# Performance work log

Hardware: AMD Instinct MI355X
Metric: run time of the kernel (lower is better)

## Reference

```python
import jax, jax.numpy as jnp
import numpy as np

N, M, NNZ, N_C, D = 4096, 4096, 262144, 4, 128
ADD_RATIO, TEMP = 0.1, 0.5


def setup_inputs() -> dict:
    key = jax.random.key(0)
    ks = jax.random.split(key, 6)
    X = jax.random.normal(ks[0], (N, D), dtype=jnp.float32)
    V = jax.random.randint(ks[1], (NNZ,), 0, N)
    E = jax.random.randint(ks[2], (NNZ,), 0, M)
    # incidence matrix consistent with the (V, E) pairs
    H = jnp.zeros((N, M), jnp.float32).at[V, E].set(1.0)
    incident_mask_prob = jax.random.uniform(ks[3], (N, M), jnp.float32, 1e-4, 1.0 - 1e-4)
    cos_weight = jax.random.normal(ks[4], (N_C, D), dtype=jnp.float32)
    eps = jax.random.uniform(ks[5], (N, M), jnp.float32, 1e-6, 1.0 - 1e-6)
    return {"X": X, "H": H, "V": V, "E": E,
            "incident_mask_prob": incident_mask_prob,
            "cos_weight": cos_weight, "eps": eps}


def _l2norm(x):
    # F.normalize(p=2, dim=-1): x / max(||x||, 1e-12)
    return x / jnp.maximum(jnp.linalg.norm(x, axis=-1, keepdims=True), 1e-12)


def reference(X, H, V, E, incident_mask_prob, cos_weight, eps):
    # scatter-mean of node embeddings into edge embeddings: eX [M, D]
    counts = jax.ops.segment_sum(jnp.ones((NNZ,), X.dtype), E, num_segments=M)
    eX = jax.ops.segment_sum(X[V], E, num_segments=M) / jnp.maximum(counts, 1.0)[:, None]

    node_fc = _l2norm(X[:, None, :] * cos_weight[None])   # [N, C, D]
    edge_fc = _l2norm(eX[:, None, :] * cos_weight[None])  # [M, C, D]
    # mean over C of per-channel cosine sims -> S [N, M]
    S = jnp.einsum('ncd,mcd->nm', node_fc, edge_fc) / N_C
    S = S.at[V, E].set(-1e30)  # mask existing incidences

    num_add = max(1, int(ADD_RATIO * NNZ))
    _, idx = jax.lax.top_k(S.reshape(-1), num_add)
    row = idx // M
    col = idx % M
    delta_H = jnp.zeros_like(H).at[row, col].set(1.0)
    enriched_H = H + delta_H

    # gumbel-sigmoid with straight-through estimator
    logit = (jnp.log(eps) - jnp.log(1.0 - eps)
             + jnp.log(incident_mask_prob + 1e-8)
             - jnp.log(1.0 - incident_mask_prob + 1e-8))
    soft = jax.nn.sigmoid(logit / TEMP)
    hard = (soft > 0.5).astype(soft.dtype)
    incident_mask = hard - jax.lax.stop_gradient(soft) + soft
    return enriched_H * incident_mask
```

## Files before the change

### kernel.cpp

```cpp
#include <hip/hip_runtime.h>

#define N_NODES 4096
#define M_EDGES 4096
#define NNZ_K   262144
#define NCH     4
#define DIM     128
#define KDIM    512
#define NM      (N_NODES * M_EDGES)
#define NUM_ADD 26214
#define NCB     2048
#define NFB     32768
#define CAP     262144
#define CAP2    65536

#define EXD_OFF   0ull
#define AFC_OFF   4194304ull
#define BFC_OFF   8388608ull
#define BKT_OFF   12582912ull
#define CVAL_OFF  13631488ull
#define CIDX_OFF  15728640ull
#define CIDX2_OFF 16777216ull
#define CNT_OFF   17039360ull
#define OFFS_OFF  17055744ull
#define CUR_OFF   17072132ull
#define HIST_OFF  17088516ull
#define FHIST_OFF 17096708ull
#define SCL_OFF   17227780ull
#define ZERO_BYTES (17227844ull - CNT_OFF)
#define NINV_OFF  17227904ull
#define EINV_OFF  17358976ull

typedef short bf16x8 __attribute__((ext_vector_type(8)));
typedef float f32x4  __attribute__((ext_vector_type(4)));

#define GLOAD_LDS16(gsrc, ldst)                                                 \
    __builtin_amdgcn_global_load_lds(                                           \
        (const __attribute__((address_space(1))) void*)(gsrc),                  \
        (__attribute__((address_space(3))) void*)(ldst), 16, 0, 0)

__device__ __forceinline__ int bin_c(float s) {
    int b = (int)floorf((s + 1.0f) * 1024.0f);
    return min(max(b, 0), NCB - 1);
}

__device__ __forceinline__ int fbin_of(double v, int bstar) {
    double lo = (double)(bstar - 12) * (2.0 / 2048.0) - 1.0;
    double wd = (28.0 * (2.0 / 2048.0)) / (double)NFB;
    int f = (int)floor((v - lo) / wd);
    return min(max(f, 0), NFB - 1);
}

__device__ __forceinline__ float hard_mask(float p, float e) {
    float logit = logf(e) - logf(1.0f - e) + logf(p + 1e-8f) - logf(1.0f - p + 1e-8f);
    float soft  = 1.0f / (1.0f + expf(-2.0f * logit));
    return (soft > 0.5f) ? 1.0f : 0.0f;
}

__device__ __forceinline__ unsigned short to_bf16_rtne(float f) {
    unsigned int b = __float_as_uint(f);
    b += 0x7FFFu + ((b >> 16) & 1u);
    return (unsigned short)(b >> 16);
}

__global__ void k_count(const int* __restrict__ E, int* __restrict__ cnt) {
    int k = blockIdx.x * 256 + threadIdx.x;
    if (k < NNZ_K) atomicAdd(&cnt[E[k]], 1);
}

__global__ __launch_bounds__(256) void k_scan(const int* __restrict__ cnt, int* __restrict__ offs) {
    __shared__ int part[256];
    int t = threadIdx.x;
    int loc[16]; int s = 0;
    for (int j = 0; j < 16; ++j) { loc[j] = cnt[t * 16 + j]; s += loc[j]; }
    part[t] = s;
    __syncthreads();
    if (t == 0) { int acc = 0; for (int i = 0; i < 256; ++i) { int v = part[i]; part[i] = acc; acc += v; } }
    __syncthreads();
    int acc = part[t];
    for (int j = 0; j < 16; ++j) { offs[t * 16 + j] = acc; acc += loc[j]; }
    if (t == 255) offs[4096] = acc;
}

__global__ void k_fill(const int* __restrict__ E, const int* __restrict__ offs,
                       int* __restrict__ cur, int* __restrict__ bkt) {
    int k = blockIdx.x * 256 + threadIdx.x;
    if (k < NNZ_K) {
        int e = E[k];
        int pos = atomicAdd(&cur[e], 1);
        bkt[offs[e] + pos] = k;
    }
}

__global__ __launch_bounds__(128) void k_edge_mean(
        const int* __restrict__ Vv, const int* __restrict__ cnt,
        const int* __restrict__ offs, const int* __restrict__ bkt,
        const float* __restrict__ X, double* __restrict__ eXd) {
    __shared__ int sk[1024];
    __shared__ int sv[1024];
    int m = blockIdx.x;
    int c = cnt[m]; if (c > 1024) c = 1024;
    int off = offs[m];
    for (int t = threadIdx.x; t < c; t += 128) sk[t] = bkt[off + t];
    __syncthreads();
    for (int t = threadIdx.x; t < c; t += 128) {
        int key = sk[t]; int r = 0;
        for (int j = 0; j < c; ++j) r += (sk[j] < key);
        sv[r] = Vv[key];
    }
    __syncthreads();
    int d = threadIdx.x;
    double s = 0.0;
    for (int j = 0; j < c; ++j) s += (double)X[sv[j] * DIM + d];
    eXd[m * DIM + d] = s / (double)(c > 1 ? c : 1);
}

template <typename T>
__global__ __launch_bounds__(128) void k_fc(const T* __restrict__ in,
                                            const float* __restrict__ w,
                                            unsigned short* __restrict__ out,
                                            double* __restrict__ dinv) {
    __shared__ double red[128];
    int n = blockIdx.x, d = threadIdx.x;
    double x = (double)in[n * DIM + d];
    for (int c = 0; c < NCH; ++c) {
        double v = x * (double)w[c * DIM + d];
        red[d] = v * v;
        __syncthreads();
        for (int s = 64; s > 0; s >>= 1) { if (d < s) red[d] += red[d + s]; __syncthreads(); }
        double denom = fmax(sqrt(red[0]), 1e-12);
        __syncthreads();
        out[n * KDIM + c * DIM + d] = to_bf16_rtne((float)(v / denom));
        if (d == 0) dinv[n * NCH + c] = 1.0 / denom;
    }
}

__global__ __launch_bounds__(256) void k_gemm_mfma(const unsigned short* __restrict__ A,
                                                   const unsigned short* __restrict__ B,
                                                   float* __restrict__ S) {
    __shared__ short As[128][32];
    __shared__ short Bs[128][32];
    int tid = threadIdx.x;
    int row0 = blockIdx.y * 128, col0 = blockIdx.x * 128;
    int w = tid >> 6, l = tid & 63;
    int wr = (w >> 1) * 64, wc = (w & 1) * 64;
    f32x4 acc[4][4] = {};
    int lrow = l >> 2, lcol = (l & 3) * 8;
    int rb0 = (w * 2 + 0) * 16, rb1 = (w * 2 + 1) * 16;
    const unsigned short* sA0 = A + (size_t)(row0 + rb0 + lrow) * KDIM + lcol;
    const unsigned short* sA1 = A + (size_t)(row0 + rb1 + lrow) * KDIM + lcol;
    const unsigned short* sB0 = B + (size_t)(col0 + rb0 + lrow) * KDIM + lcol;
    const unsigned short* sB1 = B + (size_t)(col0 + rb1 + lrow) * KDIM + lcol;
    for (int k0 = 0; k0 < KDIM; k0 += 32) {
        __syncthreads();
        GLOAD_LDS16(sA0 + k0, &As[rb0][0]);
        GLOAD_LDS16(sA1 + k0, &As[rb1][0]);
        GLOAD_LDS16(sB0 + k0, &Bs[rb0][0]);
        GLOAD_LDS16(sB1 + k0, &Bs[rb1][0]);
        __syncthreads();
        int kq = (l >> 4) * 8;
        bf16x8 af[4], bfr[4];
        #pragma unroll
        for (int m = 0; m < 4; ++m) af[m] = *(const bf16x8*)&As[wr + m * 16 + (l & 15)][kq];
        #pragma unroll
        for (int n = 0; n < 4; ++n) bfr[n] = *(const bf16x8*)&Bs[wc + n * 16 + (l & 15)][kq];
        #pragma unroll
        for (int m = 0; m < 4; ++m)
            #pragma unroll
            for (int n = 0; n < 4; ++n)
                acc[m][n] = __builtin_amdgcn_mfma_f32_16x16x32_bf16(af[m], bfr[n], acc[m][n], 0, 0, 0);
    }
    #pragma unroll
    for (int m = 0; m < 4; ++m) {
        int r = row0 + wr + m * 16 + (l >> 4) * 4;
        #pragma unroll
        for (int n = 0; n < 4; ++n) {
            int c = col0 + wc + n * 16 + (l & 15);
            #pragma unroll
            for (int j = 0; j < 4; ++j)
                S[(size_t)(r + j) * M_EDGES + c] = 0.25f * acc[m][n][j];
        }
    }
}

__global__ void k_mask(const int* __restrict__ Vv, const int* __restrict__ E,
                       float* __restrict__ S) {
    int k = blockIdx.x * 256 + threadIdx.x;
    if (k < NNZ_K) S[(size_t)Vv[k] * M_EDGES + E[k]] = -1e30f;
}

__global__ __launch_bounds__(256) void k_hist_coarse(const float4* __restrict__ S4,
                                                     int* __restrict__ hist) {
    __shared__ int h[4][NCB + 8];
    int t = threadIdx.x;
    for (int i = t; i < 4 * (NCB + 8); i += 256) ((int*)h)[i] = 0;
    __syncthreads();
    int* hc = h[t & 3];
    int stride = gridDim.x * 256;
    for (int i = blockIdx.x * 256 + t; i < NM / 4; i += stride) {
        float4 v = S4[i];
        if (v.x > -2.0f) atomicAdd(&hc[bin_c(v.x)], 1);
        if (v.y > -2.0f) atomicAdd(&hc[bin_c(v.y)], 1);
        if (v.z > -2.0f) atomicAdd(&hc[bin_c(v.z)], 1);
        if (v.w > -2.0f) atomicAdd(&hc[bin_c(v.w)], 1);
    }
    __syncthreads();
    for (int i = t; i < NCB; i += 256) {
        int s = h[0][i] + h[1][i] + h[2][i] + h[3][i];
        if (s) atomicAdd(&hist[i], s);
    }
}

__global__ __launch_bounds__(256) void k_findcut(const int* __restrict__ hist, int* __restrict__ scl) {
    __shared__ int part[256];
    __shared__ int sb;
    int t = threadIdx.x;
    int loc[8]; int s = 0;
    for (int j = 0; j < 8; ++j) { loc[j] = hist[t * 8 + j]; s += loc[j]; }
    part[t] = s;
    __syncthreads();
    if (t == 0) { int acc = 0; for (int i = 255; i >= 0; --i) { int v = part[i]; part[i] = acc; acc += v; } }
    __syncthreads();
    int run = part[t];
    for (int j = 7; j >= 0; --j) {
        int h = loc[j];
        run += h;
        if (run >= NUM_ADD && run - h < NUM_ADD) { scl[0] = t * 8 + j; sb = t * 8 + j; }
    }
    __syncthreads();
    int bstar = sb;
    int g = 0;
    for (int i = bstar + 11 + t; i < NCB; i += 256) g += hist[i];
    part[t] = g;
    __syncthreads();
    for (int st2 = 128; st2 > 0; st2 >>= 1) { if (t < st2) part[t] += part[t + st2]; __syncthreads(); }
    if (t == 0) scl[1] = part[0];
}

#define LB1 4096
#define LB2 2048
__global__ __launch_bounds__(256) void k_collect(const float4* __restrict__ S4,
        int* __restrict__ scl, int* __restrict__ cidx, int* __restrict__ cidx2) {
    __shared__ int buf1[LB1];
    __shared__ int buf2[LB2];
    __shared__ int c1, c2, g1, g2;
    int t = threadIdx.x;
    if (t == 0) { c1 = 0; c2 = 0; }
    __syncthreads();
    int bstar = scl[0];
    const int total4 = NM / 4;
    for (int i0 = blockIdx.x * 256; i0 < total4; i0 += gridDim.x * 256) {
        if (c1 > LB1 - 1024 || c2 > LB2 - 1024) {
            if (t == 0) { g1 = atomicAdd(&scl[2], c1); g2 = atomicAdd(&scl[3], c2); }
            __syncthreads();
            for (int j = t; j < c1; j += 256) { int g = g1 + j; if (g < CAP)  cidx[g]  = buf1[j]; }
            for (int j = t; j < c2; j += 256) { int g = g2 + j; if (g < CAP2) cidx2[g] = buf2[j]; }
            __syncthreads();
            if (t == 0) { c1 = 0; c2 = 0; }
            __syncthreads();
        }
        int i = i0 + t;
        if (i < total4) {
            float4 v = S4[i];
            float sc;
            #define COLLECT1(comp, cc)                                         \
                sc = comp;                                                     \
                if (sc > -2.0f) {                                              \
                    int b = bin_c(sc);                                         \
                    if (b >= bstar + 11) {                                     \
                        int s2 = atomicAdd(&c2, 1);                            \
                        buf2[s2] = i * 4 + cc;                                 \
                    } else if (b >= bstar - 11) {                              \
                        int s1 = atomicAdd(&c1, 1);                            \
                        buf1[s1] = i * 4 + cc;                                 \
                    }                                                          \
                }
            COLLECT1(v.x, 0) COLLECT1(v.y, 1) COLLECT1(v.z, 2) COLLECT1(v.w, 3)
            #undef COLLECT1
        }
        __syncthreads();
    }
    if (t == 0) { g1 = atomicAdd(&scl[2], c1); g2 = atomicAdd(&scl[3], c2); }
    __syncthreads();
    for (int j = t; j < c1; j += 256) { int g = g1 + j; if (g < CAP)  cidx[g]  = buf1[j]; }
    for (int j = t; j < c2; j += 256) { int g = g2 + j; if (g < CAP2) cidx2[g] = buf2[j]; }
}

__global__ void k_scatter(const int* __restrict__ Vv, const int* __restrict__ E,
                          const float* __restrict__ prob, const float* __restrict__ eps,
                          float* __restrict__ out) {
    int k = blockIdx.x * 256 + threadIdx.x;
    if (k < NNZ_K) {
        size_t idx = (size_t)Vv[k] * M_EDGES + E[k];
        out[idx] = hard_mask(prob[idx], eps[idx]);
    }
}

__global__ __launch_bounds__(256) void k_selc(const int* __restrict__ scl,
        const int* __restrict__ cidx2,
        const float* __restrict__ prob, const float* __restrict__ eps,
        float* __restrict__ out) {
    int n = scl[3]; if (n > CAP2) n = CAP2;
    for (int i = blockIdx.x * 256 + threadIdx.x; i < n; i += 256 * 128) {
        int idx = cidx2[i];
        out[idx] = hard_mask(prob[idx], eps[idx]);
    }
}

__global__ __launch_bounds__(256) void k_exact(
        const int* __restrict__ scl, const int* __restrict__ cidx, double* __restrict__ cval,
        const float* __restrict__ X, const double* __restrict__ eXd, const float* __restrict__ cw,
        const double* __restrict__ ninv, const double* __restrict__ einv) {
    int nc = scl[2]; if (nc > CAP) nc = CAP;
    int wid = (blockIdx.x * 256 + threadIdx.x) >> 6;
    int l = threadIdx.x & 63;
    int nw = gridDim.x * 4;
    double w2[NCH][2];
    #pragma unroll
    for (int c = 0; c < NCH; ++c) {
        float2 wc2 = *(const float2*)&cw[c * DIM + 2 * l];
        w2[c][0] = (double)wc2.x * (double)wc2.x;
        w2[c][1] = (double)wc2.y * (double)wc2.y;
    }
    for (int i = wid; i < nc; i += nw) {
        int idx = cidx[i];
        int n = idx >> 12, m = idx & (M_EDGES - 1);
        float2  x2 = *(const float2*)&X[n * DIM + 2 * l];
        double2 e2 = *(const double2*)&eXd[m * DIM + 2 * l];
        double p0 = (double)x2.x * e2.x;
        double p1 = (double)x2.y * e2.y;
        double dt0 = p0 * w2[0][0] + p1 * w2[0][1];
        double dt1 = p0 * w2[1][0] + p1 * w2[1][1];
        double dt2 = p0 * w2[2][0] + p1 * w2[2][1];
        double dt3 = p0 * w2[3][0] + p1 * w2[3][1];
        #pragma unroll
        for (int s = 1; s < 64; s <<= 1) {
            dt0 += __shfl_xor(dt0, s);
            dt1 += __shfl_xor(dt1, s);
            dt2 += __shfl_xor(dt2, s);
            dt3 += __shfl_xor(dt3, s);
        }
        if (l == 0) {
            const double* nv = &ninv[n * NCH];
            const double* ev = &einv[m * NCH];
            cval[i] = 0.25 * (dt0 * nv[0] * ev[0] + dt1 * nv[1] * ev[1]
                            + dt2 * nv[2] * ev[2] + dt3 * nv[3] * ev[3]);
        }
    }
}

__global__ __launch_bounds__(256) void k_fhist(const int* __restrict__ scl,
                                               const int* __restrict__ cidx,
                                               const double* __restrict__ cval,
                                               int* __restrict__ fh) {
    int nc = scl[2]; if (nc > CAP) nc = CAP;
    int bstar = scl[0];
    for (int i = blockIdx.x * 256 + threadIdx.x; i < nc; i += 256 * 256)
        atomicAdd(&fh[fbin_of(cval[i], bstar)], 1);
}

__global__ __launch_bounds__(1024) void k_ffind(const int* __restrict__ fh, int* __restrict__ scl) {
    __shared__ int part[1024];
    int T = NUM_ADD - scl[1];
    int t = threadIdx.x;
    int loc[32]; int s = 0;
    for (int j = 0; j < 32; ++j) { loc[j] = fh[t * 32 + j]; s += loc[j]; }
    part[t] = s;
    __syncthreads();
    if (t == 0) { int acc = 0; for (int i = 1023; i >= 0; --i) { int v = part[i]; part[i] = acc; acc += v; } }
    __syncthreads();
    int run = part[t];
    for (int j = 31; j >= 0; --j) {
        int h = loc[j];
        run += h;
        if (run >= T && run - h < T) { scl[4] = t * 32 + j; scl[5] = run - h; }
    }
}

__global__ __launch_bounds__(256) void k_write(
        const int* __restrict__ scl, const int* __restrict__ cidx, const double* __restrict__ cval,
        const float* __restrict__ prob, const float* __restrict__ eps,
        float* __restrict__ out) {
    int nc = scl[2]; if (nc > CAP) nc = CAP;
    int fs = scl[4], bstar = scl[0];
    for (int i = blockIdx.x * 256 + threadIdx.x; i < nc; i += 256 * 256) {
        if (fbin_of(cval[i], bstar) > fs) {
            int idx = cidx[i];
            out[idx] = hard_mask(prob[idx], eps[idx]);
        }
    }
}

__global__ __launch_bounds__(256) void k_tie(
        const int* __restrict__ scl, const int* __restrict__ cidx, const double* __restrict__ cval,
        const float* __restrict__ prob, const float* __restrict__ eps,
        float* __restrict__ out) {
    __shared__ double mv[256];
    __shared__ int    mi[256];
    __shared__ int    cnt;
    int nc = scl[2]; if (nc > CAP) nc = CAP;
    int T = NUM_ADD - scl[1];
    int fs = scl[4], G1f = scl[5], bstar = scl[0];
    int t = threadIdx.x;
    if (t == 0) cnt = 0;
    __syncthreads();
    for (int i = t; i < nc; i += 256) {
        if (fbin_of(cval[i], bstar) == fs) {
            int s = atomicAdd(&cnt, 1);
            if (s < 256) { mv[s] = cval[i]; mi[s] = cidx[i]; }
        }
    }
    __syncthreads();
    int nm = min(cnt, 256);
    for (int k = t; k < nm; k += 256) {
        double v = mv[k]; int idx = mi[k];
        int rank = G1f;
        for (int j = 0; j < nm; ++j)
            rank += (mv[j] > v || (mv[j] == v && mi[j] < idx)) ? 1 : 0;
        if (rank < T)
            out[idx] = hard_mask(prob[idx], eps[idx]);
    }
}

extern "C" void kernel_launch(void* const* d_in, const int* in_sizes, int n_in,
                              void* d_out, int out_size, void* d_ws, size_t ws_size,
                              hipStream_t stream) {
    const float* X    = (const float*)d_in[0];
    const int*   Vv   = (const int*)d_in[2];
    const int*   E    = (const int*)d_in[3];
    const float* prob = (const float*)d_in[4];
    const float* cw   = (const float*)d_in[5];
    const float* eps  = (const float*)d_in[6];
    float* out = (float*)d_out;
    char*  ws  = (char*)d_ws;

    double*         eXd   = (double*)(ws + EXD_OFF);
    unsigned short* Afc   = (unsigned short*)(ws + AFC_OFF);
    unsigned short* Bfc   = (unsigned short*)(ws + BFC_OFF);
    int*            bkt   = (int*)(ws + BKT_OFF);
    double*         cval  = (double*)(ws + CVAL_OFF);
    int*            cidx  = (int*)(ws + CIDX_OFF);
    int*            cidx2 = (int*)(ws + CIDX2_OFF);
    int*            cnt   = (int*)(ws + CNT_OFF);
    int*            offs  = (int*)(ws + OFFS_OFF);
    int*            cur   = (int*)(ws + CUR_OFF);
    int*            hist  = (int*)(ws + HIST_OFF);
    int*            fh    = (int*)(ws + FHIST_OFF);
    int*            scl   = (int*)(ws + SCL_OFF);
    double*         ninv  = (double*)(ws + NINV_OFF);
    double*         einv  = (double*)(ws + EINV_OFF);

    hipMemsetAsync(ws + CNT_OFF, 0, (size_t)ZERO_BYTES, stream);

    k_count<<<NNZ_K / 256, 256, 0, stream>>>(E, cnt);
    k_scan<<<1, 256, 0, stream>>>(cnt, offs);
    k_fill<<<NNZ_K / 256, 256, 0, stream>>>(E, offs, cur, bkt);
    k_edge_mean<<<M_EDGES, 128, 0, stream>>>(Vv, cnt, offs, bkt, X, eXd);
    k_fc<float><<<N_NODES, 128, 0, stream>>>(X, cw, Afc, ninv);
    k_fc<double><<<M_EDGES, 128, 0, stream>>>(eXd, cw, Bfc, einv);
    dim3 gg(M_EDGES / 128, N_NODES / 128);
    k_gemm_mfma<<<gg, 256, 0, stream>>>(Afc, Bfc, out);
    k_mask<<<NNZ_K / 256, 256, 0, stream>>>(Vv, E, out);
    k_hist_coarse<<<1024, 256, 0, stream>>>((const float4*)out, hist);
    k_findcut<<<1, 256, 0, stream>>>(hist, scl);
    k_collect<<<2048, 256, 0, stream>>>((const float4*)out, scl, cidx, cidx2);
    hipMemsetAsync(out, 0, (size_t)NM * sizeof(float), stream);
    k_scatter<<<NNZ_K / 256, 256, 0, stream>>>(Vv, E, prob, eps, out);
    k_selc<<<128, 256, 0, stream>>>(scl, cidx2, prob, eps, out);
    k_exact<<<1024, 256, 0, stream>>>(scl, cidx, cval, X, eXd, cw, ninv, einv);
    k_fhist<<<256, 256, 0, stream>>>(scl, cidx, cval, fh);
    k_ffind<<<1, 1024, 0, stream>>>(fh, scl);
    k_write<<<256, 256, 0, stream>>>(scl, cidx, cval, prob, eps, out);
    k_tie<<<1, 256, 0, stream>>>(scl, cidx, cval, prob, eps, out);
}
```

Measured before the change: 304.2 us.

## Fuse output zeroing into candidate collection and pack global counters atomically

The collect kernel now handles a fixed 4096-float chunk per block (4096 blocks, four float4 loads per thread) with no grid-stride loop or mid-loop flushes. After reading its scores it writes zeros back to the same locations, which replaces the separate full-matrix memset. The two per-block global counter atomics become one 64-bit atomic on a packed pair stored at a relocated, 8-byte-aligned counter slot. This avoids a second 64 MB pass over the output and cuts synchronisation overhead. The cost is that the shared buffers must hold every candidate a block finds in its chunk, and there is no overflow guard.

```diff
diff --git a/kernel.cpp b/kernel.cpp
--- a/kernel.cpp
+++ b/kernel.cpp
@@ -25,8 +25,8 @@
 #define CUR_OFF   17072132ull
 #define HIST_OFF  17088516ull
 #define FHIST_OFF 17096708ull
-#define SCL_OFF   17227780ull
-#define ZERO_BYTES (17227844ull - CNT_OFF)
+#define SCL_OFF   17227784ull
+#define ZERO_BYTES (17227848ull - CNT_OFF)
 #define NINV_OFF  17227904ull
 #define EINV_OFF  17358976ull
 
@@ -236,51 +236,46 @@
     if (t == 0) scl[1] = part[0];
 }
 
-#define LB1 4096
-#define LB2 2048
-__global__ __launch_bounds__(256) void k_collect(const float4* __restrict__ S4,
+#define CLB 4096
+__global__ __launch_bounds__(256) void k_collect(float4* __restrict__ S4,
         int* __restrict__ scl, int* __restrict__ cidx, int* __restrict__ cidx2) {
-    __shared__ int buf1[LB1];
-    __shared__ int buf2[LB2];
-    __shared__ int c1, c2, g1, g2;
+    __shared__ int buf1[CLB];
+    __shared__ int buf2[CLB];
+    __shared__ int c1, c2;
+    __shared__ unsigned long long gbase;
     int t = threadIdx.x;
     if (t == 0) { c1 = 0; c2 = 0; }
     __syncthreads();
     int bstar = scl[0];
-    const int total4 = NM / 4;
-    for (int i0 = blockIdx.x * 256; i0 < total4; i0 += gridDim.x * 256) {
-        if (c1 > LB1 - 1024 || c2 > LB2 - 1024) {
-            if (t == 0) { g1 = atomicAdd(&scl[2], c1); g2 = atomicAdd(&scl[3], c2); }
-            __syncthreads();
-            for (int j = t; j < c1; j += 256) { int g = g1 + j; if (g < CAP)  cidx[g]  = buf1[j]; }
-            for (int j = t; j < c2; j += 256) { int g = g2 + j; if (g < CAP2) cidx2[g] = buf2[j]; }
-            __syncthreads();
-            if (t == 0) { c1 = 0; c2 = 0; }
-            __syncthreads();
-        }
-        int i = i0 + t;
-        if (i < total4) {
-            float4 v = S4[i];
-            float sc;
-            #define COLLECT1(comp, cc)                                         \
-                sc = comp;                                                     \
-                if (sc > -2.0f) {                                              \
-                    int b = bin_c(sc);                                         \
-                    if (b >= bstar + 11) {                                     \
-                        int s2 = atomicAdd(&c2, 1);                            \
-                        buf2[s2] = i * 4 + cc;                                 \
-                    } else if (b >= bstar - 11) {                              \
-                        int s1 = atomicAdd(&c1, 1);                            \
-                        buf1[s1] = i * 4 + cc;                                 \
-                    }                                                          \
-                }
-            COLLECT1(v.x, 0) COLLECT1(v.y, 1) COLLECT1(v.z, 2) COLLECT1(v.w, 3)
-            #undef COLLECT1
-        }
-        __syncthreads();
-    }
-    if (t == 0) { g1 = atomicAdd(&scl[2], c1); g2 = atomicAdd(&scl[3], c2); }
-    __syncthreads();
+    size_t base = (size_t)blockIdx.x * 1024 + t;
+    float4 v0 = S4[base];
+    float4 v1 = S4[base + 256];
+    float4 v2 = S4[base + 512];
+    float4 v3 = S4[base + 768];
+    #define COLLECT1(sc, elem)                                                 \
+        if ((sc) > -2.0f) {                                                    \
+            int b = bin_c(sc);                                                 \
+            if (b >= bstar + 11)      buf2[atomicAdd(&c2, 1)] = (elem);        \
+            else if (b >= bstar - 11) buf1[atomicAdd(&c1, 1)] = (elem);        \
+        }
+    #define COLLECT4(v, p)                                                     \
+        COLLECT1((v).x, (int)((p) * 4 + 0)) COLLECT1((v).y, (int)((p) * 4 + 1))\
+        COLLECT1((v).z, (int)((p) * 4 + 2)) COLLECT1((v).w, (int)((p) * 4 + 3))
+    COLLECT4(v0, base) COLLECT4(v1, base + 256)
+    COLLECT4(v2, base + 512) COLLECT4(v3, base + 768)
+    #undef COLLECT4
+    #undef COLLECT1
+    float4 z = make_float4(0.f, 0.f, 0.f, 0.f);
+    S4[base] = z; S4[base + 256] = z; S4[base + 512] = z; S4[base + 768] = z;
+    __syncthreads();
+    if (t == 0) {
+        unsigned long long pack = (unsigned long long)(unsigned)c1
+                                | ((unsigned long long)(unsigned)c2 << 32);
+        gbase = atomicAdd((unsigned long long*)&scl[8], pack);
+    }
+    __syncthreads();
+    int g1 = (int)(gbase & 0xffffffffull);
+    int g2 = (int)(gbase >> 32);
     for (int j = t; j < c1; j += 256) { int g = g1 + j; if (g < CAP)  cidx[g]  = buf1[j]; }
     for (int j = t; j < c2; j += 256) { int g = g2 + j; if (g < CAP2) cidx2[g] = buf2[j]; }
 }
@@ -299,7 +294,7 @@
         const int* __restrict__ cidx2,
         const float* __restrict__ prob, const float* __restrict__ eps,
         float* __restrict__ out) {
-    int n = scl[3]; if (n > CAP2) n = CAP2;
+    int n = scl[9]; if (n > CAP2) n = CAP2;
     for (int i = blockIdx.x * 256 + threadIdx.x; i < n; i += 256 * 128) {
         int idx = cidx2[i];
         out[idx] = hard_mask(prob[idx], eps[idx]);
@@ -310,7 +305,7 @@
         const int* __restrict__ scl, const int* __restrict__ cidx, double* __restrict__ cval,
         const float* __restrict__ X, const double* __restrict__ eXd, const float* __restrict__ cw,
         const double* __restrict__ ninv, const double* __restrict__ einv) {
-    int nc = scl[2]; if (nc > CAP) nc = CAP;
+    int nc = scl[8]; if (nc > CAP) nc = CAP;
     int wid = (blockIdx.x * 256 + threadIdx.x) >> 6;
     int l = threadIdx.x & 63;
     int nw = gridDim.x * 4;
@@ -352,7 +347,7 @@
                                                const int* __restrict__ cidx,
                                                const double* __restrict__ cval,
                                                int* __restrict__ fh) {
-    int nc = scl[2]; if (nc > CAP) nc = CAP;
+    int nc = scl[8]; if (nc > CAP) nc = CAP;
     int bstar = scl[0];
     for (int i = blockIdx.x * 256 + threadIdx.x; i < nc; i += 256 * 256)
         atomicAdd(&fh[fbin_of(cval[i], bstar)], 1);
@@ -380,7 +375,7 @@
         const int* __restrict__ scl, const int* __restrict__ cidx, const double* __restrict__ cval,
         const float* __restrict__ prob, const float* __restrict__ eps,
         float* __restrict__ out) {
-    int nc = scl[2]; if (nc > CAP) nc = CAP;
+    int nc = scl[8]; if (nc > CAP) nc = CAP;
     int fs = scl[4], bstar = scl[0];
     for (int i = blockIdx.x * 256 + threadIdx.x; i < nc; i += 256 * 256) {
         if (fbin_of(cval[i], bstar) > fs) {
@@ -397,7 +392,7 @@
     __shared__ double mv[256];
     __shared__ int    mi[256];
     __shared__ int    cnt;
-    int nc = scl[2]; if (nc > CAP) nc = CAP;
+    int nc = scl[8]; if (nc > CAP) nc = CAP;
     int T = NUM_ADD - scl[1];
     int fs = scl[4], G1f = scl[5], bstar = scl[0];
     int t = threadIdx.x;
@@ -462,8 +457,7 @@
     k_mask<<<NNZ_K / 256, 256, 0, stream>>>(Vv, E, out);
     k_hist_coarse<<<1024, 256, 0, stream>>>((const float4*)out, hist);
     k_findcut<<<1, 256, 0, stream>>>(hist, scl);
-    k_collect<<<2048, 256, 0, stream>>>((const float4*)out, scl, cidx, cidx2);
-    hipMemsetAsync(out, 0, (size_t)NM * sizeof(float), stream);
+    k_collect<<<4096, 256, 0, stream>>>((float4*)out, scl, cidx, cidx2);
     k_scatter<<<NNZ_K / 256, 256, 0, stream>>>(Vv, E, prob, eps, out);
     k_selc<<<128, 256, 0, stream>>>(scl, cidx2, prob, eps, out);
     k_exact<<<1024, 256, 0, stream>>>(scl, cidx, cval, X, eXd, cw, ninv, einv);
```

After: 296.5 us. 2.5% less time.
